# Performance work log

Hardware: AMD Instinct MI355X
Metric: run time of the kernel (lower is better)

## Reference

```python
import jax, jax.numpy as jnp
import numpy as np

NEG = -9.0e15
BN_EPS = 1e-5


def _build_graph():
    N = 22
    A = np.eye(N, dtype=np.float32)
    for i in range(N - 1):
        A[i, i + 1] = 1.0
        A[i + 1, i] = 1.0
    distal = [3, 7, 11, 15, 16, 20, 21]
    jl = [0, 1, 2, 3, 17, 18, 19, 20, 21]
    jr = [4, 5, 6, 7, 12, 13, 14, 15, 16]
    adj_sym = np.zeros((N, N), dtype=np.float32)
    for i in range(N):
        adj_sym[i, i] = 1.0
        if i in jl:
            adj_sym[i, jr[jl.index(i)]] = 1.0
        if i in jr:
            adj_sym[i, jl[jr.index(i)]] = 1.0
    A1 = A.copy()
    for i in distal:
        A1[i] = 0.0
    A2 = np.linalg.matrix_power(A, 2)
    A3 = np.linalg.matrix_power(A, 3)
    for i in range(N):
        if i not in distal:
            A2[i] = 0.0
            A3[i] = 0.0
    adj_con = A1 + A2 + A3
    return adj_sym, adj_con


def setup_inputs() -> dict:
    key = jax.random.key(0)
    B, T, N, C, O = 64, 50, 22, 64, 64
    adj_sym, adj_con = _build_graph()
    rs, cs = np.nonzero(adj_sym > 0)  # row-major, matches torch nonzero order
    rc, cc = np.nonzero(adj_con > 0)
    ks = jax.random.split(key, 11)
    f32 = jnp.float32
    return {
        "x": jax.random.normal(ks[0], (B, T, N, C), f32),
        "W_sym": 0.1 * jax.random.normal(ks[1], (2, C, O), f32),
        "e_sym": 1.0 + 0.1 * jax.random.normal(ks[2], (O, len(rs)), f32),
        "W_con": 0.1 * jax.random.normal(ks[3], (2, C, O), f32),
        "e_con": 1.0 + 0.1 * jax.random.normal(ks[4], (O, len(rc)), f32),
        "W_dis": 0.1 * jax.random.normal(ks[5], (C, O), f32),
        "att": 0.1 * jax.random.normal(ks[6], (N, N), f32),
        "b_dis": 0.1 * jax.random.normal(ks[7], (O,), f32),
        "cat_w": 0.05 * jax.random.normal(ks[8], (O, 3 * O), f32),
        "gammas": 1.0 + 0.1 * jax.random.normal(ks[9], (4, O), f32),
        "betas": 0.1 * jax.random.normal(ks[10], (4, O), f32),
        "rows_sym": jnp.asarray(rs, jnp.int32),
        "cols_sym": jnp.asarray(cs, jnp.int32),
        "rows_con": jnp.asarray(rc, jnp.int32),
        "cols_con": jnp.asarray(cc, jnp.int32),
    }


def _semch(x, W, e, rows, cols):
    # x: [B,T,N,C], W: [2,C,O], e: [O,nnz] -> [B,T,N,O]
    N = x.shape[2]
    O = W.shape[2]
    h0 = x @ W[0]  # [B,T,N,O]
    h1 = x @ W[1]
    logits = jnp.full((O, N, N), NEG, x.dtype).at[:, rows, cols].set(e)
    A = jax.nn.softmax(logits, axis=2)  # per-channel masked softmax over rows
    diag = A[:, jnp.arange(N), jnp.arange(N)]  # [O,N]
    A_off = A * (1.0 - jnp.eye(N, dtype=x.dtype))
    return h0 * diag.T[None, None] + jnp.einsum('cij,btjc->btic', A_off, h1)


def _bn_relu(h, g, b):
    # training-mode BatchNorm2d over [B,C,T,N], stats on (0,2,3)
    mu = h.mean(axis=(0, 2, 3), keepdims=True)
    var = ((h - mu) ** 2).mean(axis=(0, 2, 3), keepdims=True)
    out = (h - mu) * jax.lax.rsqrt(var + BN_EPS) * g[None, :, None, None] + b[None, :, None, None]
    return jax.nn.relu(out)


def reference(x, W_sym, e_sym, W_con, e_con, W_dis, att, b_dis, cat_w,
              gammas, betas, rows_sym, cols_sym, rows_con, cols_con):
    xs = _semch(x, W_sym, e_sym, rows_sym, cols_sym)  # [B,T,N,O]
    yc = _semch(x, W_con, e_con, rows_con, cols_con)  # [B,T,N,O]
    # pairwise distance branch: pos_rel [B,T,N,N,C], summed over dim 2
    pos_rel = x[:, :, :, None, :] - x[:, :, None, :, :]
    dis = jnp.sqrt(jnp.sum(pos_rel * pos_rel, axis=2)) + 1e-8  # [B,T,N,C]
    z = jnp.einsum('ij,btjo->btio', att, dis @ W_dis) + b_dis  # GraphConvolution
    # to NCHW: [B,O,T,N]
    xp = _bn_relu(xs.transpose(0, 3, 1, 2), gammas[0], betas[0])
    yp = _bn_relu(yc.transpose(0, 3, 1, 2), gammas[1], betas[1])
    zp = _bn_relu(z.transpose(0, 3, 1, 2), gammas[2], betas[2])
    cat = jnp.concatenate((xp, yp, zp), axis=1)  # [B,3O,T,N]
    out = jnp.einsum('of,bftn->botn', cat_w, cat)  # 1x1 conv
    out = _bn_relu(out, gammas[3], betas[3])
    return out.transpose(0, 2, 3, 1)  # [B,T,N,O]
```

## Files before the change

### kernel.cpp

```cpp
#include <hip/hip_runtime.h>
#include <hip/hip_bf16.h>

typedef __hip_bfloat16 bf16;
typedef __attribute__((ext_vector_type(8))) short bf16x8;
typedef __attribute__((ext_vector_type(4))) float f32x4;

#define BT    3200
#define N_    22
#define NO    1408
#define NN    484
#define BTN   70400
#define ELEMS 4505600
#define MAXNZ 128

static __device__ __forceinline__ bf16  f2bf(float v) { return __float2bfloat16(v); }
static __device__ __forceinline__ short fbf(float v) {
    bf16 h = __float2bfloat16(v);
    return *reinterpret_cast<short*>(&h);
}
static __device__ __forceinline__ float sbf(short s) {
    return __uint_as_float(((unsigned)(unsigned short)s) << 16);
}
static __device__ __forceinline__ void unp(unsigned u, float& lo, float& hi) {
    lo = __uint_as_float(u << 16);
    hi = __uint_as_float(u & 0xffff0000u);
}

__global__ void prep_kernel(const float* __restrict__ e_s, const int* __restrict__ rs,
                            const int* __restrict__ cs, int nnz_s,
                            const float* __restrict__ e_c, const int* __restrict__ rc,
                            const int* __restrict__ cc, int nnz_c,
                            const float* __restrict__ cat_w,
                            const float* __restrict__ Wsym, const float* __restrict__ Wcon,
                            const float* __restrict__ Wdis,
                            short* __restrict__ AAb, short* __restrict__ CB,
                            short* __restrict__ WB) {
    const int tid = threadIdx.x;
    if (blockIdx.x < 2) {
        __shared__ float eL[64 * (MAXNZ + 1)];
        __shared__ int rowsL[MAXNZ], colsL[MAXNZ];
        const int t = blockIdx.x;
        const float* e    = t ? e_c : e_s;
        const int*   rows = t ? rc  : rs;
        const int*   cols = t ? cc  : cs;
        const int    nnz  = t ? nnz_c : nnz_s;
        const int    str  = nnz + 1;

        for (int idx = tid; idx < 64 * nnz; idx += 256) {
            int o = idx / nnz, k = idx - o * nnz;
            eL[o * str + k] = expf(e[idx]);
        }
        for (int idx = tid; idx < nnz; idx += 256) { rowsL[idx] = rows[idx]; colsL[idx] = cols[idx]; }
        __syncthreads();

        const int o = tid & 63, ig = tid >> 6;
        float s[6];
        #pragma unroll
        for (int q = 0; q < 6; q++) s[q] = 0.f;
        for (int k = 0; k < nnz; k++) {
            int r = rowsL[k];
            float ev = eL[o * str + k];
            #pragma unroll
            for (int q = 0; q < 6; q++)
                if (r == ig + 4 * q) s[q] += ev;
        }
        float inv[6];
        #pragma unroll
        for (int q = 0; q < 6; q++) inv[q] = 1.f / s[q];
        for (int k = 0; k < nnz; k++) {
            int r = rowsL[k];
            #pragma unroll
            for (int q = 0; q < 6; q++)
                if (r == ig + 4 * q)
                    AAb[((size_t)(r * N_ + colsL[k]) * 64 + o) * 2 + t] =
                        fbf(eL[o * str + k] * inv[q]);
        }
    } else if (blockIdx.x < 8) {
        int gi = (blockIdx.x - 2) * 256 + tid;
        if (gi >= 1536) return;
        int nt = gi / 384, rem = gi % 384;
        int kc = rem >> 6, L = rem & 63;
        int n = nt * 16 + (L & 15);
        int kbase = kc * 32 + (L >> 4) * 8;
        float4 w0 = *(const float4*)&cat_w[n * 192 + kbase];
        float4 w1 = *(const float4*)&cat_w[n * 192 + kbase + 4];
        bf16x8 frag;
        frag[0] = fbf(w0.x); frag[1] = fbf(w0.y); frag[2] = fbf(w0.z); frag[3] = fbf(w0.w);
        frag[4] = fbf(w1.x); frag[5] = fbf(w1.y); frag[6] = fbf(w1.z); frag[7] = fbf(w1.w);
        ((bf16x8*)CB)[gi] = frag;
    } else {
        int gi = (blockIdx.x - 8) * 256 + tid;
        if (gi >= 2560) return;
        int L = gi & 63;
        int q = gi >> 6;
        int nt = q & 3;
        int pk = q >> 2;
        int kc = pk & 1;
        int p  = pk >> 1;
        const float* Wsrc = (p == 0) ? Wsym :
                            (p == 1) ? Wsym + 4096 :
                            (p == 2) ? Wcon :
                            (p == 3) ? Wcon + 4096 : Wdis;
        int n  = nt * 16 + (L & 15);
        int kb = kc * 32 + (L >> 4) * 8;
        bf16x8 frag;
        #pragma unroll
        for (int j = 0; j < 8; j++) frag[j] = fbf(Wsrc[(kb + j) * 64 + n]);
        ((bf16x8*)WB)[gi] = frag;
    }
}

__launch_bounds__(256)
__global__ void pre_pass(const float* __restrict__ x,
                         bf16* __restrict__ xb, bf16* __restrict__ db) {
    __shared__ float xt[4 * NO];
    const int tid = threadIdx.x;
    const int w = tid >> 6, L = tid & 63;
    const size_t base = (size_t)blockIdx.x * 4 * NO;
    for (int idx = tid; idx < NO; idx += 256)
        ((float4*)xt)[idx] = ((const float4*)(x + base))[idx];
    __syncthreads();
    const float* xw = xt + w * NO;
    float s = 0.f, s2 = 0.f;
    #pragma unroll
    for (int i = 0; i < N_; i++) { float v = xw[i * 64 + L]; s += v; s2 += v * v; }
    const size_t wb = base + (size_t)w * NO;
    #pragma unroll
    for (int i = 0; i < N_; i++) {
        float v  = xw[i * 64 + L];
        float d2 = s2 - 2.f * v * s + (float)N_ * v * v;
        float d  = sqrtf(fmaxf(d2, 0.f)) + 1e-8f;
        xb[wb + i * 64 + L] = f2bf(v);
        db[wb + i * 64 + L] = f2bf(d);
    }
}

__launch_bounds__(256)
__global__ void fused_hmix(const bf16* __restrict__ xb, const bf16* __restrict__ db,
                           const short* __restrict__ WB, const short* __restrict__ AAb,
                           const float* __restrict__ att, const float* __restrict__ bdis,
                           bf16* __restrict__ xs, bf16* __restrict__ yc,
                           bf16* __restrict__ z, float* __restrict__ stats1) {
    __shared__ __align__(16) unsigned pp0[2 * NO];
    __shared__ __align__(16) unsigned pp1[2 * NO];
    __shared__ __align__(16) short p2[2 * NO];
    __shared__ float attL[NN];
    float* red = (float*)pp0;

    const int g   = blockIdx.x;
    const int tid = threadIdx.x;
    const size_t base = (size_t)g * 2 * NO;
    const int w = tid >> 6, L = tid & 63;
    const int lane16 = L & 15, quad = L >> 4;
    const bf16x8* WBf = (const bf16x8*)WB;

    for (int idx = tid; idx < NN; idx += 256) attL[idx] = att[idx];

    f32x4 acc[5][3];
    #pragma unroll
    for (int p = 0; p < 5; p++)
        #pragma unroll
        for (int rt = 0; rt < 3; rt++) acc[p][rt] = (f32x4){0.f, 0.f, 0.f, 0.f};

    #pragma unroll
    for (int kc = 0; kc < 2; kc++) {
        bf16x8 ax[3], ad[3];
        #pragma unroll
        for (int rt = 0; rt < 3; rt++) {
            int gr = g * 44 + rt * 16 + lane16;
            if (gr > BTN - 1) gr = BTN - 1;
            ax[rt] = *(const bf16x8*)(xb + (size_t)gr * 64 + kc * 32 + quad * 8);
            ad[rt] = *(const bf16x8*)(db + (size_t)gr * 64 + kc * 32 + quad * 8);
        }
        #pragma unroll
        for (int p = 0; p < 5; p++) {
            bf16x8 bw = WBf[((p * 2 + kc) * 4 + w) * 64 + L];
            #pragma unroll
            for (int rt = 0; rt < 3; rt++) {
                bf16x8 a = (p < 4) ? ax[rt] : ad[rt];
                acc[p][rt] = __builtin_amdgcn_mfma_f32_16x16x32_bf16(a, bw, acc[p][rt], 0, 0, 0);
            }
        }
    }

    {
        int col = w * 16 + lane16;
        #pragma unroll
        for (int rt = 0; rt < 3; rt++)
            #pragma unroll
            for (int r = 0; r < 4; r++) {
                int m = rt * 16 + quad * 4 + r;
                if (m < 44) {
                    float h0s = acc[0][rt][r], h1s = acc[1][rt][r];
                    float h0c = acc[2][rt][r], h1c = acc[3][rt][r];
                    pp0[m * 64 + col] = (unsigned)(unsigned short)fbf(h1s) |
                                        ((unsigned)(unsigned short)fbf(h0s - h1s) << 16);
                    pp1[m * 64 + col] = (unsigned)(unsigned short)fbf(h1c) |
                                        ((unsigned)(unsigned short)fbf(h0c - h1c) << 16);
                    p2[m * 64 + col] = fbf(acc[4][rt][r]);
                }
            }
    }
    __syncthreads();

    float mxs[2][6], myc[2][6], mz[2][6];
    #pragma unroll
    for (int b = 0; b < 2; b++)
        #pragma unroll
        for (int k = 0; k < 6; k++) { mxs[b][k] = myc[b][k] = mz[b][k] = 0.f; }

    const unsigned* AAu = (const unsigned*)AAb;
    for (int j = 0; j < N_; j++) {
        float h1s[2], h1c[2], hw[2], dum;
        #pragma unroll
        for (int b = 0; b < 2; b++) {
            unp(pp0[b * NO + j * 64 + L], h1s[b], dum);
            unp(pp1[b * NO + j * 64 + L], h1c[b], dum);
            hw[b] = sbf(p2[b * NO + j * 64 + L]);
        }
        #pragma unroll
        for (int k = 0; k < 6; k++) {
            int i  = w + 4 * k;
            int ii = (i < N_) ? i : 0;
            unsigned a = AAu[(size_t)(ii * N_ + j) * 64 + L];
            float as, ac; unp(a, as, ac);
            float atv = attL[ii * N_ + j];
            #pragma unroll
            for (int b = 0; b < 2; b++) {
                mxs[b][k] = fmaf(as,  h1s[b], mxs[b][k]);
                myc[b][k] = fmaf(ac,  h1c[b], myc[b][k]);
                mz[b][k]  = fmaf(atv, hw[b],  mz[b][k]);
            }
        }
    }

    float bd = bdis[L];
    float st0 = 0.f, st1 = 0.f, st2 = 0.f, st3 = 0.f, st4 = 0.f, st5 = 0.f;
    #pragma unroll
    for (int k = 0; k < 6; k++) {
        int i = w + 4 * k;
        if (i < N_) {
            unsigned ad = AAu[(size_t)(i * 23) * 64 + L];
            float asd, acd; unp(ad, asd, acd);
            #pragma unroll
            for (int b = 0; b < 2; b++) {
                float dum, dsv, dcv;
                unp(pp0[b * NO + i * 64 + L], dum, dsv);
                unp(pp1[b * NO + i * 64 + L], dum, dcv);
                float xsv = mxs[b][k] + asd * dsv;
                float ycv = myc[b][k] + acd * dcv;
                float zv  = mz[b][k] + bd;
                size_t oi = base + b * NO + i * 64 + L;
                xs[oi] = f2bf(xsv); yc[oi] = f2bf(ycv); z[oi] = f2bf(zv);
                st0 += xsv; st1 += xsv * xsv;
                st2 += ycv; st3 += ycv * ycv;
                st4 += zv;  st5 += zv  * zv;
            }
        }
    }

    __syncthreads();
    red[(w * 6 + 0) * 64 + L] = st0;
    red[(w * 6 + 1) * 64 + L] = st1;
    red[(w * 6 + 2) * 64 + L] = st2;
    red[(w * 6 + 3) * 64 + L] = st3;
    red[(w * 6 + 4) * 64 + L] = st4;
    red[(w * 6 + 5) * 64 + L] = st5;
    __syncthreads();
    float* myStats = stats1 + (size_t)(g & 7) * 384;
    for (int qq = tid; qq < 384; qq += 256) {
        int q = qq >> 6, oo = qq & 63;
        float v = (red[q * 64 + oo] + red[(6 + q) * 64 + oo]) +
                  (red[(12 + q) * 64 + oo] + red[(18 + q) * 64 + oo]);
        atomicAdd(&myStats[qq], v);
    }
}

__global__ void scale_from_stats(const float* __restrict__ stats,
                                 const float* __restrict__ gammas,
                                 const float* __restrict__ betas,
                                 int nch, int gbase, int nshard, int sstride,
                                 float* __restrict__ scale) {
    int tid = threadIdx.x;
    if (tid >= nch * 64) return;
    int t = tid >> 6, o = tid & 63;
    float S = 0.f, SS = 0.f;
    for (int s = 0; s < nshard; s++) {
        S  += stats[s * sstride + (2 * t) * 64 + o];
        SS += stats[s * sstride + (2 * t + 1) * 64 + o];
    }
    const float invn = 1.f / (float)BTN;
    float mu   = S * invn;
    float var  = SS * invn - mu * mu;
    float rstd = rsqrtf(var + 1e-5f);
    float a = gammas[(gbase + t) * 64 + o] * rstd;
    float c = betas[(gbase + t) * 64 + o] - mu * a;
    scale[t * 128 + o]      = a;
    scale[t * 128 + 64 + o] = c;
}

__launch_bounds__(256)
__global__ void mix_pass(const bf16* __restrict__ xs, const bf16* __restrict__ yc,
                         const bf16* __restrict__ z, const float* __restrict__ scale1,
                         const short* __restrict__ CB,
                         bf16* __restrict__ out2, float* __restrict__ stats2) {
    __shared__ float sL[384];
    __shared__ float red[512];

    const int tid = threadIdx.x;
    const int w = tid >> 6, L = tid & 63;
    const int lane16 = L & 15, quad = L >> 4;
    const int R0 = blockIdx.x * 128 + w * 32;

    for (int idx = tid; idx < 384; idx += 256) sL[idx] = scale1[idx];
    __syncthreads();

    const bf16* srcs[3] = { xs, yc, z };

    f32x4 acc[2][4];
    #pragma unroll
    for (int rt = 0; rt < 2; rt++)
        #pragma unroll
        for (int nt = 0; nt < 4; nt++)
            acc[rt][nt] = (f32x4){0.f, 0.f, 0.f, 0.f};

    #pragma unroll
    for (int kc = 0; kc < 6; kc++) {
        const int src = kc >> 1;
        const int c0  = (kc & 1) * 32 + quad * 8;
        bf16x8 av[2];
        #pragma unroll
        for (int rt = 0; rt < 2; rt++) {
            int row = R0 + rt * 16 + lane16;
            uint4 u = *(const uint4*)(srcs[src] + (size_t)row * 64 + c0);
            float v[8];
            unp(u.x, v[0], v[1]); unp(u.y, v[2], v[3]);
            unp(u.z, v[4], v[5]); unp(u.w, v[6], v[7]);
            #pragma unroll
            for (int e = 0; e < 8; e++) {
                float t = fmaxf(fmaf(v[e], sL[src * 128 + c0 + e],
                                     sL[src * 128 + 64 + c0 + e]), 0.f);
                av[rt][e] = fbf(t);
            }
        }
        #pragma unroll
        for (int nt = 0; nt < 4; nt++) {
            bf16x8 bw = ((const bf16x8*)CB)[(nt * 6 + kc) * 64 + L];
            acc[0][nt] = __builtin_amdgcn_mfma_f32_16x16x32_bf16(av[0], bw, acc[0][nt], 0, 0, 0);
            acc[1][nt] = __builtin_amdgcn_mfma_f32_16x16x32_bf16(av[1], bw, acc[1][nt], 0, 0, 0);
        }
    }

    float s[4]  = {0.f, 0.f, 0.f, 0.f};
    float s2[4] = {0.f, 0.f, 0.f, 0.f};
    #pragma unroll
    for (int rt = 0; rt < 2; rt++)
        #pragma unroll
        for (int nt = 0; nt < 4; nt++)
            #pragma unroll
            for (int r = 0; r < 4; r++) {
                int row = R0 + rt * 16 + quad * 4 + r;
                int col = nt * 16 + lane16;
                float v = acc[rt][nt][r];
                out2[(size_t)row * 64 + col] = f2bf(v);
                s[nt] += v; s2[nt] += v * v;
            }
    #pragma unroll
    for (int nt = 0; nt < 4; nt++) {
        s[nt]  += __shfl_xor(s[nt], 16);
        s[nt]  += __shfl_xor(s[nt], 32);
        s2[nt] += __shfl_xor(s2[nt], 16);
        s2[nt] += __shfl_xor(s2[nt], 32);
    }
    if (quad == 0) {
        #pragma unroll
        for (int nt = 0; nt < 4; nt++) {
            red[w * 64 + nt * 16 + lane16]       = s[nt];
            red[256 + w * 64 + nt * 16 + lane16] = s2[nt];
        }
    }
    __syncthreads();
    if (tid < 64) {
        float t = red[tid] + red[64 + tid] + red[128 + tid] + red[192 + tid];
        atomicAdd(&stats2[tid], t);
    } else if (tid < 128) {
        int c = tid - 64;
        float t = red[256 + c] + red[320 + c] + red[384 + c] + red[448 + c];
        atomicAdd(&stats2[64 + c], t);
    }
}

__global__ void final_pass(const bf16* __restrict__ out2, const float* __restrict__ scale2,
                           float* __restrict__ out) {
    const int gid = blockIdx.x * 256 + threadIdx.x;
    const int idx = gid * 4;
    ushort4 u = reinterpret_cast<const ushort4*>(out2)[gid];
    const int o = idx & 63;
    float f0, f1, f2, f3;
    unp((unsigned)u.x | ((unsigned)u.y << 16), f0, f1);
    unp((unsigned)u.z | ((unsigned)u.w << 16), f2, f3);
    float4 r;
    r.x = fmaxf(fmaf(f0, scale2[o],     scale2[64 + o]),     0.f);
    r.y = fmaxf(fmaf(f1, scale2[o + 1], scale2[64 + o + 1]), 0.f);
    r.z = fmaxf(fmaf(f2, scale2[o + 2], scale2[64 + o + 2]), 0.f);
    r.w = fmaxf(fmaf(f3, scale2[o + 3], scale2[64 + o + 3]), 0.f);
    reinterpret_cast<float4*>(out)[gid] = r;
}

extern "C" void kernel_launch(void* const* d_in, const int* in_sizes, int n_in,
                              void* d_out, int out_size, void* d_ws, size_t ws_size,
                              hipStream_t stream) {
    const float* x      = (const float*)d_in[0];
    const float* W_sym  = (const float*)d_in[1];
    const float* e_sym  = (const float*)d_in[2];
    const float* W_con  = (const float*)d_in[3];
    const float* e_con  = (const float*)d_in[4];
    const float* W_dis  = (const float*)d_in[5];
    const float* att    = (const float*)d_in[6];
    const float* b_dis  = (const float*)d_in[7];
    const float* cat_w  = (const float*)d_in[8];
    const float* gammas = (const float*)d_in[9];
    const float* betas  = (const float*)d_in[10];
    const int* rows_sym = (const int*)d_in[11];
    const int* cols_sym = (const int*)d_in[12];
    const int* rows_con = (const int*)d_in[13];
    const int* cols_con = (const int*)d_in[14];
    const int nnz_s = in_sizes[2] / 64;
    const int nnz_c = in_sizes[4] / 64;

    char* p = (char*)d_ws;
    float* stats  = (float*)p; p += (8 * 384 + 128) * 4;
    float* scale1 = (float*)p; p += 384 * 4;
    float* scale2 = (float*)p; p += 128 * 4;
    short* AAb    = (short*)p; p += (size_t)NN * 64 * 2 * 2;
    short* CB     = (short*)p; p += (size_t)1536 * 8 * 2;
    short* WB     = (short*)p; p += (size_t)2560 * 8 * 2;
    bf16*  xb     = (bf16*)p;  p += (size_t)ELEMS * 2;
    bf16*  db     = (bf16*)p;  p += (size_t)ELEMS * 2;
    bf16*  xsb    = (bf16*)p;  p += (size_t)ELEMS * 2;
    bf16*  ycb    = (bf16*)p;  p += (size_t)ELEMS * 2;
    bf16*  zb     = (bf16*)p;  p += (size_t)ELEMS * 2;
    bf16*  out2   = xb;
    float* stats1 = stats;
    float* stats2 = stats + 8 * 384;

    hipMemsetAsync(stats, 0, (8 * 384 + 128) * 4, stream);
    hipMemsetAsync(AAb, 0, (size_t)NN * 64 * 2 * 2, stream);
    prep_kernel<<<18, 256, 0, stream>>>(e_sym, rows_sym, cols_sym, nnz_s,
                                        e_con, rows_con, cols_con, nnz_c,
                                        cat_w, W_sym, W_con, W_dis, AAb, CB, WB);
    pre_pass<<<800, 256, 0, stream>>>(x, xb, db);
    fused_hmix<<<1600, 256, 0, stream>>>(xb, db, WB, AAb, att, b_dis,
                                         xsb, ycb, zb, stats1);
    scale_from_stats<<<1, 192, 0, stream>>>(stats1, gammas, betas, 3, 0, 8, 384, scale1);
    mix_pass<<<550, 256, 0, stream>>>(xsb, ycb, zb, scale1, CB, out2, stats2);
    scale_from_stats<<<1, 64, 0, stream>>>(stats2, gammas, betas, 1, 3, 1, 0, scale2);
    final_pass<<<ELEMS / 1024, 256, 0, stream>>>(out2, scale2, (float*)d_out);
}
```

Baseline: 204.2 us.

## Fuse distance pre-pass into hmix kernel and use MFMA and sparsity for mixing

```diff
diff --git a/kernel.cpp b/kernel.cpp
--- a/kernel.cpp
+++ b/kernel.cpp
@@ -5,13 +5,14 @@
 typedef __attribute__((ext_vector_type(8))) short bf16x8;
 typedef __attribute__((ext_vector_type(4))) float f32x4;
 
-#define BT    3200
-#define N_    22
-#define NO    1408
-#define NN    484
-#define BTN   70400
-#define ELEMS 4505600
-#define MAXNZ 128
+#define BT     3200
+#define N_     22
+#define NO     1408
+#define NN     484
+#define BTN    70400
+#define ELEMS  4505600
+#define MAXNZ  128
+#define NSHARD 16
 
 static __device__ __forceinline__ bf16  f2bf(float v) { return __float2bfloat16(v); }
 static __device__ __forceinline__ short fbf(float v) {
@@ -32,9 +33,10 @@
                             const int* __restrict__ cc, int nnz_c,
                             const float* __restrict__ cat_w,
                             const float* __restrict__ Wsym, const float* __restrict__ Wcon,
-                            const float* __restrict__ Wdis,
+                            const float* __restrict__ Wdis, const float* __restrict__ att,
                             short* __restrict__ AAb, short* __restrict__ CB,
-                            short* __restrict__ WB) {
+                            short* __restrict__ WB, int* __restrict__ bm,
+                            short* __restrict__ attF) {
     const int tid = threadIdx.x;
     if (blockIdx.x < 2) {
         __shared__ float eL[64 * (MAXNZ + 1)];
@@ -88,7 +90,7 @@
         frag[0] = fbf(w0.x); frag[1] = fbf(w0.y); frag[2] = fbf(w0.z); frag[3] = fbf(w0.w);
         frag[4] = fbf(w1.x); frag[5] = fbf(w1.y); frag[6] = fbf(w1.z); frag[7] = fbf(w1.w);
         ((bf16x8*)CB)[gi] = frag;
-    } else {
+    } else if (blockIdx.x < 18) {
         int gi = (blockIdx.x - 8) * 256 + tid;
         if (gi >= 2560) return;
         int L = gi & 63;
@@ -107,172 +109,219 @@
         #pragma unroll
         for (int j = 0; j < 8; j++) frag[j] = fbf(Wsrc[(kb + j) * 64 + n]);
         ((bf16x8*)WB)[gi] = frag;
+    } else {
+        if (tid < N_) {
+            unsigned bits = 0u;
+            for (int e = 0; e < nnz_s; e++)
+                if (rs[e] == tid && cs[e] != tid) bits |= 1u << cs[e];
+            for (int e = 0; e < nnz_c; e++)
+                if (rc[e] == tid && cc[e] != tid) bits |= 1u << cc[e];
+            bm[tid] = (int)bits;
+        }
+        for (int f = tid; f < 128; f += 256) {
+            int rt = f >> 6, LL = f & 63;
+            int row = rt * 16 + (LL & 15);
+            int kb  = (LL >> 4) * 8;
+            bf16x8 frag;
+            #pragma unroll
+            for (int j = 0; j < 8; j++) {
+                int k = kb + j;
+                float vv = (row < N_ && k < N_) ? att[row * N_ + k] : 0.f;
+                frag[j] = fbf(vv);
+            }
+            ((bf16x8*)attF)[f] = frag;
+        }
     }
 }
 
 __launch_bounds__(256)
-__global__ void pre_pass(const float* __restrict__ x,
-                         bf16* __restrict__ xb, bf16* __restrict__ db) {
-    __shared__ float xt[4 * NO];
-    const int tid = threadIdx.x;
-    const int w = tid >> 6, L = tid & 63;
-    const size_t base = (size_t)blockIdx.x * 4 * NO;
-    for (int idx = tid; idx < NO; idx += 256)
-        ((float4*)xt)[idx] = ((const float4*)(x + base))[idx];
-    __syncthreads();
-    const float* xw = xt + w * NO;
-    float s = 0.f, s2 = 0.f;
-    #pragma unroll
-    for (int i = 0; i < N_; i++) { float v = xw[i * 64 + L]; s += v; s2 += v * v; }
-    const size_t wb = base + (size_t)w * NO;
-    #pragma unroll
-    for (int i = 0; i < N_; i++) {
-        float v  = xw[i * 64 + L];
-        float d2 = s2 - 2.f * v * s + (float)N_ * v * v;
-        float d  = sqrtf(fmaxf(d2, 0.f)) + 1e-8f;
-        xb[wb + i * 64 + L] = f2bf(v);
-        db[wb + i * 64 + L] = f2bf(d);
-    }
-}
-
-__launch_bounds__(256)
-__global__ void fused_hmix(const bf16* __restrict__ xb, const bf16* __restrict__ db,
-                           const short* __restrict__ WB, const short* __restrict__ AAb,
-                           const float* __restrict__ att, const float* __restrict__ bdis,
+__global__ void fused_hmix(const float* __restrict__ x, const short* __restrict__ WB,
+                           const short* __restrict__ AAb, const short* __restrict__ attF,
+                           const int* __restrict__ bm, const float* __restrict__ bdis,
                            bf16* __restrict__ xs, bf16* __restrict__ yc,
                            bf16* __restrict__ z, float* __restrict__ stats1) {
-    __shared__ __align__(16) unsigned pp0[2 * NO];
-    __shared__ __align__(16) unsigned pp1[2 * NO];
-    __shared__ __align__(16) short p2[2 * NO];
-    __shared__ float attL[NN];
-    float* red = (float*)pp0;
+    __shared__ __align__(16) char smem[14080];
+    short*    xl   = (short*)smem;
+    short*    dl   = (short*)(smem + 4096);
+    float*    red4 = (float*)(smem + 8192);
+    unsigned* pp0  = (unsigned*)smem;
+    unsigned* pp1  = (unsigned*)(smem + 5632);
+    short*    p2   = (short*)(smem + 11264);
+    float*    red  = (float*)smem;
 
     const int g   = blockIdx.x;
     const int tid = threadIdx.x;
-    const size_t base = (size_t)g * 2 * NO;
+    const size_t base = (size_t)g * NO;
     const int w = tid >> 6, L = tid & 63;
     const int lane16 = L & 15, quad = L >> 4;
+    const int colw = w * 16 + lane16;
     const bf16x8* WBf = (const bf16x8*)WB;
 
-    for (int idx = tid; idx < NN; idx += 256) attL[idx] = att[idx];
-
-    f32x4 acc[5][3];
+    float v[6], s = 0.f, s2 = 0.f;
+    #pragma unroll
+    for (int k = 0; k < 6; k++) {
+        int i = w + 4 * k;
+        float t = (i < N_) ? x[base + i * 64 + L] : 0.f;
+        v[k] = t; s += t; s2 += t * t;
+    }
+    red4[w * 64 + L]       = s;
+    red4[256 + w * 64 + L] = s2;
+    for (int idx = tid; idx < 320; idx += 256) {
+        ((unsigned*)xl)[704 + idx] = 0u;
+        ((unsigned*)dl)[704 + idx] = 0u;
+    }
+    __syncthreads();
+    float S  = (red4[L] + red4[64 + L]) + (red4[128 + L] + red4[192 + L]);
+    float S2 = (red4[256 + L] + red4[320 + L]) + (red4[384 + L] + red4[448 + L]);
+    #pragma unroll
+    for (int k = 0; k < 6; k++) {
+        int i = w + 4 * k;
+        if (i < N_) {
+            float t = v[k];
+            float d2 = S2 - 2.f * t * S + (float)N_ * t * t;
+            float d  = sqrtf(fmaxf(d2, 0.f)) + 1e-8f;
+            int ci = i * 64 + (L ^ ((i & 7) << 3));
+            xl[ci] = fbf(t);
+            dl[ci] = fbf(d);
+        }
+    }
+    __syncthreads();
+
+    f32x4 acc[5][2];
     #pragma unroll
     for (int p = 0; p < 5; p++)
         #pragma unroll
-        for (int rt = 0; rt < 3; rt++) acc[p][rt] = (f32x4){0.f, 0.f, 0.f, 0.f};
+        for (int rt = 0; rt < 2; rt++) acc[p][rt] = (f32x4){0.f, 0.f, 0.f, 0.f};
 
     #pragma unroll
     for (int kc = 0; kc < 2; kc++) {
-        bf16x8 ax[3], ad[3];
-        #pragma unroll
-        for (int rt = 0; rt < 3; rt++) {
-            int gr = g * 44 + rt * 16 + lane16;
-            if (gr > BTN - 1) gr = BTN - 1;
-            ax[rt] = *(const bf16x8*)(xb + (size_t)gr * 64 + kc * 32 + quad * 8);
-            ad[rt] = *(const bf16x8*)(db + (size_t)gr * 64 + kc * 32 + quad * 8);
+        bf16x8 ax[2], ad[2];
+        #pragma unroll
+        for (int rt = 0; rt < 2; rt++) {
+            int row = rt * 16 + lane16;
+            int ci  = row * 64 + ((kc * 32 + quad * 8) ^ ((row & 7) << 3));
+            ax[rt] = *(const bf16x8*)(xl + ci);
+            ad[rt] = *(const bf16x8*)(dl + ci);
         }
         #pragma unroll
         for (int p = 0; p < 5; p++) {
             bf16x8 bw = WBf[((p * 2 + kc) * 4 + w) * 64 + L];
             #pragma unroll
-            for (int rt = 0; rt < 3; rt++) {
+            for (int rt = 0; rt < 2; rt++) {
                 bf16x8 a = (p < 4) ? ax[rt] : ad[rt];
                 acc[p][rt] = __builtin_amdgcn_mfma_f32_16x16x32_bf16(a, bw, acc[p][rt], 0, 0, 0);
             }
         }
     }
-
+    __syncthreads();
+
+    #pragma unroll
+    for (int rt = 0; rt < 2; rt++)
+        #pragma unroll
+        for (int r = 0; r < 4; r++) {
+            int m = rt * 16 + quad * 4 + r;
+            if (m < N_) {
+                float h0s = acc[0][rt][r], h1s = acc[1][rt][r];
+                float h0c = acc[2][rt][r], h1c = acc[3][rt][r];
+                pp0[m * 64 + colw] = (unsigned)(unsigned short)fbf(h1s) |
+                                     ((unsigned)(unsigned short)fbf(h0s) << 16);
+                pp1[m * 64 + colw] = (unsigned)(unsigned short)fbf(h1c) |
+                                     ((unsigned)(unsigned short)fbf(h0c) << 16);
+                p2[m * 64 + colw] = fbf(acc[4][rt][r]);
+            }
+        }
+    __syncthreads();
+
+    f32x4 zacc[2];
+    zacc[0] = (f32x4){0.f, 0.f, 0.f, 0.f};
+    zacc[1] = (f32x4){0.f, 0.f, 0.f, 0.f};
     {
-        int col = w * 16 + lane16;
-        #pragma unroll
-        for (int rt = 0; rt < 3; rt++)
-            #pragma unroll
-            for (int r = 0; r < 4; r++) {
-                int m = rt * 16 + quad * 4 + r;
-                if (m < 44) {
-                    float h0s = acc[0][rt][r], h1s = acc[1][rt][r];
-                    float h0c = acc[2][rt][r], h1c = acc[3][rt][r];
-                    pp0[m * 64 + col] = (unsigned)(unsigned short)fbf(h1s) |
-                                        ((unsigned)(unsigned short)fbf(h0s - h1s) << 16);
-                    pp1[m * 64 + col] = (unsigned)(unsigned short)fbf(h1c) |
-                                        ((unsigned)(unsigned short)fbf(h0c - h1c) << 16);
-                    p2[m * 64 + col] = fbf(acc[4][rt][r]);
-                }
-            }
-    }
-    __syncthreads();
-
-    float mxs[2][6], myc[2][6], mz[2][6];
-    #pragma unroll
-    for (int b = 0; b < 2; b++)
-        #pragma unroll
-        for (int k = 0; k < 6; k++) { mxs[b][k] = myc[b][k] = mz[b][k] = 0.f; }
-
+        bf16x8 bfrag;
+        #pragma unroll
+        for (int j = 0; j < 8; j++) {
+            int k = quad * 8 + j;
+            bfrag[j] = (k < N_) ? p2[k * 64 + colw] : (short)0;
+        }
+        const bf16x8* attFf = (const bf16x8*)attF;
+        #pragma unroll
+        for (int rt = 0; rt < 2; rt++)
+            zacc[rt] = __builtin_amdgcn_mfma_f32_16x16x32_bf16(attFf[rt * 64 + L], bfrag,
+                                                               zacc[rt], 0, 0, 0);
+    }
+
+    float mxs[6], myc[6];
+    #pragma unroll
+    for (int k = 0; k < 6; k++) { mxs[k] = 0.f; myc[k] = 0.f; }
     const unsigned* AAu = (const unsigned*)AAb;
-    for (int j = 0; j < N_; j++) {
-        float h1s[2], h1c[2], hw[2], dum;
-        #pragma unroll
-        for (int b = 0; b < 2; b++) {
-            unp(pp0[b * NO + j * 64 + L], h1s[b], dum);
-            unp(pp1[b * NO + j * 64 + L], h1c[b], dum);
-            hw[b] = sbf(p2[b * NO + j * 64 + L]);
-        }
-        #pragma unroll
-        for (int k = 0; k < 6; k++) {
-            int i  = w + 4 * k;
-            int ii = (i < N_) ? i : 0;
-            unsigned a = AAu[(size_t)(ii * N_ + j) * 64 + L];
-            float as, ac; unp(a, as, ac);
-            float atv = attL[ii * N_ + j];
-            #pragma unroll
-            for (int b = 0; b < 2; b++) {
-                mxs[b][k] = fmaf(as,  h1s[b], mxs[b][k]);
-                myc[b][k] = fmaf(ac,  h1c[b], myc[b][k]);
-                mz[b][k]  = fmaf(atv, hw[b],  mz[b][k]);
-            }
-        }
-    }
-
-    float bd = bdis[L];
-    float st0 = 0.f, st1 = 0.f, st2 = 0.f, st3 = 0.f, st4 = 0.f, st5 = 0.f;
     #pragma unroll
     for (int k = 0; k < 6; k++) {
         int i = w + 4 * k;
         if (i < N_) {
-            unsigned ad = AAu[(size_t)(i * 23) * 64 + L];
-            float asd, acd; unp(ad, asd, acd);
-            #pragma unroll
-            for (int b = 0; b < 2; b++) {
-                float dum, dsv, dcv;
-                unp(pp0[b * NO + i * 64 + L], dum, dsv);
-                unp(pp1[b * NO + i * 64 + L], dum, dcv);
-                float xsv = mxs[b][k] + asd * dsv;
-                float ycv = myc[b][k] + acd * dcv;
-                float zv  = mz[b][k] + bd;
-                size_t oi = base + b * NO + i * 64 + L;
-                xs[oi] = f2bf(xsv); yc[oi] = f2bf(ycv); z[oi] = f2bf(zv);
-                st0 += xsv; st1 += xsv * xsv;
-                st2 += ycv; st3 += ycv * ycv;
-                st4 += zv;  st5 += zv  * zv;
-            }
-        }
-    }
-
-    __syncthreads();
-    red[(w * 6 + 0) * 64 + L] = st0;
-    red[(w * 6 + 1) * 64 + L] = st1;
-    red[(w * 6 + 2) * 64 + L] = st2;
-    red[(w * 6 + 3) * 64 + L] = st3;
-    red[(w * 6 + 4) * 64 + L] = st4;
-    red[(w * 6 + 5) * 64 + L] = st5;
-    __syncthreads();
-    float* myStats = stats1 + (size_t)(g & 7) * 384;
+            unsigned bits = (unsigned)bm[i];
+            while (bits) {
+                int j = __ffs(bits) - 1;
+                bits &= bits - 1;
+                unsigned a = AAu[(size_t)(i * N_ + j) * 64 + L];
+                float as, ac; unp(a, as, ac);
+                float h1s = sbf((short)pp0[j * 64 + L]);
+                float h1c = sbf((short)pp1[j * 64 + L]);
+                mxs[k] = fmaf(as, h1s, mxs[k]);
+                myc[k] = fmaf(ac, h1c, myc[k]);
+            }
+        }
+    }
+
+    float st0 = 0.f, st1 = 0.f, st2 = 0.f, st3 = 0.f;
+    #pragma unroll
+    for (int k = 0; k < 6; k++) {
+        int i = w + 4 * k;
+        if (i < N_) {
+            unsigned ad2 = AAu[(size_t)(i * 23) * 64 + L];
+            float asd, acd; unp(ad2, asd, acd);
+            float h0sv = __uint_as_float(pp0[i * 64 + L] & 0xffff0000u);
+            float h0cv = __uint_as_float(pp1[i * 64 + L] & 0xffff0000u);
+            float xsv = mxs[k] + asd * h0sv;
+            float ycv = myc[k] + acd * h0cv;
+            size_t oi = base + i * 64 + L;
+            xs[oi] = f2bf(xsv); yc[oi] = f2bf(ycv);
+            st0 += xsv; st1 += xsv * xsv;
+            st2 += ycv; st3 += ycv * ycv;
+        }
+    }
+
+    float bd = bdis[colw];
+    float st4 = 0.f, st5 = 0.f;
+    #pragma unroll
+    for (int rt = 0; rt < 2; rt++)
+        #pragma unroll
+        for (int r = 0; r < 4; r++) {
+            int m = rt * 16 + quad * 4 + r;
+            if (m < N_) {
+                float zv = zacc[rt][r] + bd;
+                z[base + (size_t)m * 64 + colw] = f2bf(zv);
+                st4 += zv; st5 += zv * zv;
+            }
+        }
+    st4 += __shfl_xor(st4, 16); st4 += __shfl_xor(st4, 32);
+    st5 += __shfl_xor(st5, 16); st5 += __shfl_xor(st5, 32);
+
+    __syncthreads();
+    red[(w * 4 + 0) * 64 + L] = st0;
+    red[(w * 4 + 1) * 64 + L] = st1;
+    red[(w * 4 + 2) * 64 + L] = st2;
+    red[(w * 4 + 3) * 64 + L] = st3;
+    if (quad == 0) { red[16 * 64 + colw] = st4; red[17 * 64 + colw] = st5; }
+    __syncthreads();
+    float* myStats = stats1 + (size_t)(g & (NSHARD - 1)) * 384;
     for (int qq = tid; qq < 384; qq += 256) {
-        int q = qq >> 6, oo = qq & 63;
-        float v = (red[q * 64 + oo] + red[(6 + q) * 64 + oo]) +
-                  (red[(12 + q) * 64 + oo] + red[(18 + q) * 64 + oo]);
-        atomicAdd(&myStats[qq], v);
+        int q = qq >> 6, o = qq & 63;
+        float vv;
+        if (q < 4)
+            vv = (red[q * 64 + o] + red[(4 + q) * 64 + o]) +
+                 (red[(8 + q) * 64 + o] + red[(12 + q) * 64 + o]);
+        else
+            vv = red[(12 + q) * 64 + o];
+        atomicAdd(&myStats[qq], vv);
     }
 }
 
@@ -429,30 +478,30 @@
     const int nnz_c = in_sizes[4] / 64;
 
     char* p = (char*)d_ws;
-    float* stats  = (float*)p; p += (8 * 384 + 128) * 4;
+    float* stats  = (float*)p; p += (NSHARD * 384 + 128) * 4;
     float* scale1 = (float*)p; p += 384 * 4;
     float* scale2 = (float*)p; p += 128 * 4;
     short* AAb    = (short*)p; p += (size_t)NN * 64 * 2 * 2;
     short* CB     = (short*)p; p += (size_t)1536 * 8 * 2;
     short* WB     = (short*)p; p += (size_t)2560 * 8 * 2;
-    bf16*  xb     = (bf16*)p;  p += (size_t)ELEMS * 2;
-    bf16*  db     = (bf16*)p;  p += (size_t)ELEMS * 2;
+    int*   bm     = (int*)p;   p += 128;
+    short* attF   = (short*)p; p += 128 * 16;
     bf16*  xsb    = (bf16*)p;  p += (size_t)ELEMS * 2;
     bf16*  ycb    = (bf16*)p;  p += (size_t)ELEMS * 2;
     bf16*  zb     = (bf16*)p;  p += (size_t)ELEMS * 2;
-    bf16*  out2   = xb;
+    bf16*  out2   = (bf16*)p;  p += (size_t)ELEMS * 2;
     float* stats1 = stats;
-    float* stats2 = stats + 8 * 384;
-
-    hipMemsetAsync(stats, 0, (8 * 384 + 128) * 4, stream);
+    float* stats2 = stats + NSHARD * 384;
+
+    hipMemsetAsync(stats, 0, (NSHARD * 384 + 128) * 4, stream);
     hipMemsetAsync(AAb, 0, (size_t)NN * 64 * 2 * 2, stream);
-    prep_kernel<<<18, 256, 0, stream>>>(e_sym, rows_sym, cols_sym, nnz_s,
+    prep_kernel<<<19, 256, 0, stream>>>(e_sym, rows_sym, cols_sym, nnz_s,
                                         e_con, rows_con, cols_con, nnz_c,
-                                        cat_w, W_sym, W_con, W_dis, AAb, CB, WB);
-    pre_pass<<<800, 256, 0, stream>>>(x, xb, db);
-    fused_hmix<<<1600, 256, 0, stream>>>(xb, db, WB, AAb, att, b_dis,
-                                         xsb, ycb, zb, stats1);
-    scale_from_stats<<<1, 192, 0, stream>>>(stats1, gammas, betas, 3, 0, 8, 384, scale1);
+                                        cat_w, W_sym, W_con, W_dis, att,
+                                        AAb, CB, WB, bm, attF);
+    fused_hmix<<<BT, 256, 0, stream>>>(x, WB, AAb, attF, bm, b_dis,
+                                       xsb, ycb, zb, stats1);
+    scale_from_stats<<<1, 192, 0, stream>>>(stats1, gammas, betas, 3, 0, NSHARD, 384, scale1);
     mix_pass<<<550, 256, 0, stream>>>(xsb, ycb, zb, scale1, CB, out2, stats2);
     scale_from_stats<<<1, 64, 0, stream>>>(stats2, gammas, betas, 1, 3, 1, 0, scale2);
     final_pass<<<ELEMS / 1024, 256, 0, stream>>>(out2, scale2, (float*)d_out);
```

New measurement: 199.2 us. 2.5% less time.
